# Kernel tuning notes

Hardware: AMD Instinct MI355X
Metric: run time of the kernel (lower is better)

## Reference

```python
import jax, jax.numpy as jnp
import numpy as np

B, T, DIM = 32, 512, 512
Q, C, D = 8, 256, 256   # num_codebooks, nb_code, bottleneck_dim
HID = 1024
EPS = 1e-5


def _bn(h, gamma, beta):
    # BatchNorm1d (training mode): batch stats over all leading dims, biased var
    ax = tuple(range(h.ndim - 1))
    m = h.mean(axis=ax, keepdims=True)
    v = ((h - m) ** 2).mean(axis=ax, keepdims=True)
    return (h - m) / jnp.sqrt(v + EPS) * gamma + beta


def setup_inputs() -> dict:
    key = jax.random.key(0)
    ks = jax.random.split(key, 12)
    s = 0.02  # weight scale
    return {
        "x": jax.random.normal(ks[0], (B, DIM, T), jnp.float32),
        "u": jax.random.uniform(ks[1], (B, T, Q, C), jnp.float32),
        "codebook": jax.random.normal(ks[2], (Q, C, D), jnp.float32),
        "log_temps": jnp.zeros((Q,), jnp.float32),
        "enc_w0": jax.random.normal(ks[3], (HID, DIM), jnp.float32) * s,
        "enc_b0": jnp.zeros((HID,), jnp.float32),
        "enc_g0": jnp.ones((HID,), jnp.float32),
        "enc_be0": jnp.zeros((HID,), jnp.float32),
        "enc_w1": jax.random.normal(ks[4], (HID, HID), jnp.float32) * s,
        "enc_b1": jnp.zeros((HID,), jnp.float32),
        "enc_g1": jnp.ones((HID,), jnp.float32),
        "enc_be1": jnp.zeros((HID,), jnp.float32),
        "enc_wo": jax.random.normal(ks[5], (Q * D, HID), jnp.float32) * s,
        "enc_bo": jnp.zeros((Q * D,), jnp.float32),
        "dec_g": jnp.ones((D,), jnp.float32),
        "dec_be": jnp.zeros((D,), jnp.float32),
        "dec_w0": jax.random.normal(ks[6], (HID, D), jnp.float32) * s,
        "dec_b0": jnp.zeros((HID,), jnp.float32),
        "dec_g0": jnp.ones((HID,), jnp.float32),
        "dec_be0": jnp.zeros((HID,), jnp.float32),
        "dec_w1": jax.random.normal(ks[7], (HID, HID), jnp.float32) * s,
        "dec_b1": jnp.zeros((HID,), jnp.float32),
        "dec_g1": jnp.ones((HID,), jnp.float32),
        "dec_be1": jnp.zeros((HID,), jnp.float32),
        "fin_w": jax.random.normal(ks[8], (DIM, HID), jnp.float32) * s,
        "fin_b": jnp.zeros((DIM,), jnp.float32),
    }


def reference(x, u, codebook, log_temps,
              enc_w0, enc_b0, enc_g0, enc_be0,
              enc_w1, enc_b1, enc_g1, enc_be1,
              enc_wo, enc_bo,
              dec_g, dec_be,
              dec_w0, dec_b0, dec_g0, dec_be0,
              dec_w1, dec_b1, dec_g1, dec_be1,
              fin_w, fin_b):
    xt = jnp.swapaxes(x, 1, 2)  # b c t -> b t c

    # encoder: FFN(dim->hid->hid) + Linear(hid, Q*D)
    h = jax.nn.relu(_bn(xt @ enc_w0.T + enc_b0, enc_g0, enc_be0))
    h = jax.nn.relu(_bn(h @ enc_w1.T + enc_b1, enc_g1, enc_be1))
    z = (h @ enc_wo.T + enc_bo).reshape(B, T, Q, D)

    # multi-codebook logits
    logits_raw = jnp.einsum('btqd,qcd->btqc', z, codebook)  # [B,T,Q,C]
    indices = jnp.argmax(logits_raw, axis=-1)               # [B,T,Q]

    # per-codebook temperature scaling
    logits = logits_raw * jnp.exp(-log_temps)[:, None]

    # gumbel-softmax (tau=1, hard=True), gumbel noise from uniform u
    g = -jnp.log(-jnp.log(jnp.clip(u, 1e-9, 1.0)) + 1e-20)
    y_soft = jax.nn.softmax(logits + g, axis=-1)
    y_hard = jax.nn.one_hot(jnp.argmax(y_soft, axis=-1), C, dtype=y_soft.dtype)
    codes = y_hard - jax.lax.stop_gradient(y_soft) + y_soft  # straight-through

    # decoder: embed via codebook, batchnorm, FFN, final linear
    emb = codes.reshape(B, T, Q * C) @ codebook.reshape(Q * C, D)
    h = _bn(emb, dec_g, dec_be)
    h = jax.nn.relu(_bn(h @ dec_w0.T + dec_b0, dec_g0, dec_be0))
    h = jax.nn.relu(_bn(h @ dec_w1.T + dec_b1, dec_g1, dec_be1))
    x_reco = h @ fin_w.T + fin_b  # [B,T,DIM]

    commit_loss = jnp.mean((x_reco - xt) ** 2)
    return x_reco, indices, commit_loss
```

## Files before the change

kernel.cpp:

```cpp
#include <hip/hip_runtime.h>
#include <math.h>

#define BB   32
#define TT   512
#define DIM  512
#define HID  1024
#define QQ   8
#define CC   256
#define DD   256
#define BT   16384
#define EPSB 1e-5f

typedef _Float16 half4 __attribute__((ext_vector_type(4)));
typedef _Float16 half8 __attribute__((ext_vector_type(8)));
typedef float f32x4 __attribute__((ext_vector_type(4)));

#define GLOAD_LDS16(g, l)                                                      \
  __builtin_amdgcn_global_load_lds(                                            \
      (const __attribute__((address_space(1))) void*)(g),                      \
      (__attribute__((address_space(3))) void*)(l), 16, 0, 0)

__device__ inline void xcd_swizzle(int& bx, int& by) {
  int gx = gridDim.x, gy = gridDim.y;
  int h = blockIdx.x + gx * blockIdx.y;
  int c = h & 7, idx = h >> 3;
  bx = idx % gx;
  by = c * (gy >> 3) + idx / gx;
}

__global__ __launch_bounds__(256) void transpose_xt(const float* __restrict__ x,
                                                    float* __restrict__ xt,
                                                    _Float16* __restrict__ xhi,
                                                    _Float16* __restrict__ xlo) {
  __shared__ float tile[32][33];
  int tx = threadIdx.x, ty = threadIdx.y;
  int b = blockIdx.z;
  int t0 = blockIdx.x * 32, c0 = blockIdx.y * 32;
  const float* xb = x + (size_t)b * DIM * TT;
#pragma unroll
  for (int j = 0; j < 32; j += 8)
    tile[ty + j][tx] = xb[(size_t)(c0 + ty + j) * TT + (t0 + tx)];
  __syncthreads();
#pragma unroll
  for (int j = 0; j < 32; j += 8) {
    float v = tile[tx][ty + j];
    size_t gi = ((size_t)b * TT + t0 + ty + j) * DIM + (c0 + tx);
    xt[gi] = v;
    _Float16 h = (_Float16)v;
    xhi[gi] = h;
    xlo[gi] = (_Float16)(v - (float)h);
  }
}

__device__ inline void conv4(const float* __restrict__ in,
                             _Float16* __restrict__ o, int i) {
  float4 v = ((const float4*)in)[i];
  half4 hv;
  hv.x = (_Float16)v.x; hv.y = (_Float16)v.y;
  hv.z = (_Float16)v.z; hv.w = (_Float16)v.w;
  ((half4*)o)[i] = hv;
}

__device__ inline void split4(const float* __restrict__ in,
                              _Float16* __restrict__ hi,
                              _Float16* __restrict__ lo, int i, float scale) {
  float4 v = ((const float4*)in)[i];
  v.x *= scale; v.y *= scale; v.z *= scale; v.w *= scale;
  half4 hv, lv;
  hv.x = (_Float16)v.x; lv.x = (_Float16)(v.x - (float)hv.x);
  hv.y = (_Float16)v.y; lv.y = (_Float16)(v.y - (float)hv.y);
  hv.z = (_Float16)v.z; lv.z = (_Float16)(v.z - (float)hv.z);
  hv.w = (_Float16)v.w; lv.w = (_Float16)(v.w - (float)hv.w);
  ((half4*)hi)[i] = hv;
  ((half4*)lo)[i] = lv;
}

__global__ __launch_bounds__(256) void prep_weights(
    const float* __restrict__ dw0, const float* __restrict__ dw1,
    const float* __restrict__ fw, const float* __restrict__ ew0,
    const float* __restrict__ ew1, _Float16* __restrict__ w0h,
    _Float16* __restrict__ w1h, _Float16* __restrict__ wfh,
    _Float16* __restrict__ w0hi, _Float16* __restrict__ w0lo,
    _Float16* __restrict__ w1hi, _Float16* __restrict__ w1lo) {
  int b = blockIdx.x, t = threadIdx.x;
  if (b < 256) {
    conv4(dw0, w0h, b * 256 + t);
  } else if (b < 1280) {
    conv4(dw1, w1h, (b - 256) * 256 + t);
  } else if (b < 1792) {
    conv4(fw, wfh, (b - 1280) * 256 + t);
  } else if (b < 2304) {
    split4(ew0, w0hi, w0lo, (b - 1792) * 256 + t, 64.f);
  } else {
    split4(ew1, w1hi, w1lo, (b - 2304) * 256 + t, 64.f);
  }
}

__global__ __launch_bounds__(256) void fold_w(const float* __restrict__ cb,
                                              const float* __restrict__ wo,
                                              float* __restrict__ Wf) {
  __shared__ float As[8][128];
  __shared__ float Ws[8][128];
  const int tid = threadIdx.x;
  const int n0 = blockIdx.x * 128;
  const int m0 = blockIdx.y * 128;
  const int q = m0 >> 8;
  const int lr = tid >> 1, lk = (tid & 1) << 2;
  const float* Ap = cb + (size_t)q * CC * DD + (size_t)((m0 & 255) + lr) * DD + lk;
  const int br = tid >> 5, bc = (tid & 31) << 2;
  const float* Bp = wo + (size_t)(q * CC + br) * HID + n0 + bc;
  const int tm = (tid >> 4) << 3, tn = (tid & 15) << 3;

  float acc[8][8];
#pragma unroll
  for (int i = 0; i < 8; i++)
#pragma unroll
    for (int j = 0; j < 8; j++) acc[i][j] = 0.f;

  for (int kb = 0; kb < DD; kb += 8) {
    float4 av = *(const float4*)(Ap + kb);
    float4 bb = *(const float4*)(Bp + (size_t)kb * HID);
    __syncthreads();
    As[lk + 0][lr] = av.x; As[lk + 1][lr] = av.y;
    As[lk + 2][lr] = av.z; As[lk + 3][lr] = av.w;
    *(float4*)&Ws[br][bc] = bb;
    __syncthreads();
#pragma unroll
    for (int k = 0; k < 8; ++k) {
      float a[8], b[8];
      *(float4*)(a) = *(const float4*)(&As[k][tm]);
      *(float4*)(a + 4) = *(const float4*)(&As[k][tm + 4]);
      *(float4*)(b) = *(const float4*)(&Ws[k][tn]);
      *(float4*)(b + 4) = *(const float4*)(&Ws[k][tn + 4]);
#pragma unroll
      for (int i = 0; i < 8; i++)
#pragma unroll
        for (int j = 0; j < 8; j++) acc[i][j] = fmaf(a[i], b[j], acc[i][j]);
    }
  }
#pragma unroll
  for (int i = 0; i < 8; i++) {
    float* Cp = Wf + (size_t)(m0 + tm + i) * HID + (n0 + tn);
    float4 o;
    o.x = acc[i][0]; o.y = acc[i][1]; o.z = acc[i][2]; o.w = acc[i][3];
    *(float4*)Cp = o;
    o.x = acc[i][4]; o.y = acc[i][5]; o.z = acc[i][6]; o.w = acc[i][7];
    *(float4*)(Cp + 4) = o;
  }
}

__global__ __launch_bounds__(256) void fold_b(const float* __restrict__ cb,
                                              const float* __restrict__ bo,
                                              float* __restrict__ bf) {
  int q = blockIdx.x, c = threadIdx.x;
  const float* row = cb + ((size_t)q * CC + c) * DD;
  const float* b = bo + q * DD;
  float s = 0.f;
  for (int d = 0; d < DD; d++) s = fmaf(row[d], b[d], s);
  bf[q * CC + c] = s;
}

__global__ __launch_bounds__(256, 2) void hgemm3s_nt(
    const _Float16* __restrict__ Ahi, const _Float16* __restrict__ Alo,
    const _Float16* __restrict__ Whi, const _Float16* __restrict__ Wlo,
    const float* __restrict__ bias, float invsc, _Float16* __restrict__ Chi,
    _Float16* __restrict__ Clo, int ldc, int K, float* __restrict__ stats,
    int N) {
  __shared__ _Float16 Ah[4 * 128 * 8];
  __shared__ _Float16 Al[4 * 128 * 8];
  __shared__ _Float16 Bh[4 * 128 * 8];
  __shared__ _Float16 Bl[4 * 128 * 8];
  int BX, BY;
  xcd_swizzle(BX, BY);
  const int tid = threadIdx.x;
  const int l = tid & 63;
  const int w = tid >> 6;
  const int m0 = BY * 128, n0 = BX * 128;
  const int wrow = (w >> 1) * 64, wcol = (w & 1) * 64;

  const int s0 = tid, s1 = tid + 256;
  const int r0 = s0 & 127, kp0 = s0 >> 7;
  const int r1 = s1 & 127, kp1 = s1 >> 7;
  const size_t a0o = (size_t)(m0 + r0) * K + kp0 * 8;
  const size_t a1o = (size_t)(m0 + r1) * K + kp1 * 8;
  const size_t w0o = (size_t)(n0 + r0) * K + kp0 * 8;
  const size_t w1o = (size_t)(n0 + r1) * K + kp1 * 8;

  f32x4 acc[4][4] = {};

  for (int kb = 0; kb < K; kb += 32) {
    __syncthreads();
    GLOAD_LDS16(Ahi + a0o + kb, &Ah[s0 * 8]);
    GLOAD_LDS16(Ahi + a1o + kb, &Ah[s1 * 8]);
    GLOAD_LDS16(Alo + a0o + kb, &Al[s0 * 8]);
    GLOAD_LDS16(Alo + a1o + kb, &Al[s1 * 8]);
    GLOAD_LDS16(Whi + w0o + kb, &Bh[s0 * 8]);
    GLOAD_LDS16(Whi + w1o + kb, &Bh[s1 * 8]);
    GLOAD_LDS16(Wlo + w0o + kb, &Bl[s0 * 8]);
    GLOAD_LDS16(Wlo + w1o + kb, &Bl[s1 * 8]);
    __syncthreads();
    half8 ah[4], al[4], bh[4], bl[4];
#pragma unroll
    for (int i = 0; i < 4; i++) {
      const int idx = (((l >> 4) << 7) + wrow + i * 16 + (l & 15)) * 8;
      ah[i] = *(const half8*)&Ah[idx];
      al[i] = *(const half8*)&Al[idx];
    }
#pragma unroll
    for (int j = 0; j < 4; j++) {
      const int idx = (((l >> 4) << 7) + wcol + j * 16 + (l & 15)) * 8;
      bh[j] = *(const half8*)&Bh[idx];
      bl[j] = *(const half8*)&Bl[idx];
    }
#pragma unroll
    for (int i = 0; i < 4; i++)
#pragma unroll
      for (int j = 0; j < 4; j++) {
        acc[i][j] = __builtin_amdgcn_mfma_f32_16x16x32_f16(ah[i], bh[j],
                                                           acc[i][j], 0, 0, 0);
        acc[i][j] = __builtin_amdgcn_mfma_f32_16x16x32_f16(al[i], bh[j],
                                                           acc[i][j], 0, 0, 0);
        acc[i][j] = __builtin_amdgcn_mfma_f32_16x16x32_f16(ah[i], bl[j],
                                                           acc[i][j], 0, 0, 0);
      }
  }

#pragma unroll
  for (int j = 0; j < 4; j++) {
    const int col = n0 + wcol + j * 16 + (l & 15);
    const float bb = bias[col];
    float s1v = 0.f, s2v = 0.f;
#pragma unroll
    for (int i = 0; i < 4; i++) {
#pragma unroll
      for (int r = 0; r < 4; r++) {
        float v = fmaf(acc[i][j][r], invsc, bb);
        const int row = m0 + wrow + i * 16 + ((l >> 4) << 2) + r;
        _Float16 hv = (_Float16)v;
        Chi[(size_t)row * ldc + col] = hv;
        Clo[(size_t)row * ldc + col] = (_Float16)(v - (float)hv);
        s1v += v;
        s2v = fmaf(v, v, s2v);
      }
    }
    s1v += __shfl_xor(s1v, 16); s1v += __shfl_xor(s1v, 32);
    s2v += __shfl_xor(s2v, 16); s2v += __shfl_xor(s2v, 32);
    if (l < 16) {
      atomicAdd(&stats[col], s1v);
      atomicAdd(&stats[N + col], s2v);
    }
  }
}

__global__ __launch_bounds__(512, 4) void hgemm3_wo_argmax(
    const _Float16* __restrict__ Ahi, const _Float16* __restrict__ Alo,
    const _Float16* __restrict__ Whi, const _Float16* __restrict__ Wlo,
    const float* __restrict__ bf, const float* __restrict__ u,
    const float* __restrict__ log_temps, float* __restrict__ out_idx,
    int* __restrict__ idx2) {
  __shared__ _Float16 Ahs[4 * 128 * 8];
  __shared__ _Float16 Als[4 * 128 * 8];
  __shared__ _Float16 Bhs[4 * 256 * 8];
  __shared__ _Float16 Bls[4 * 256 * 8];
  __shared__ float redv[2][128][4];
  __shared__ int   redi[2][128][4];
  int BX, BY;
  xcd_swizzle(BX, BY);
  const int tid = threadIdx.x;
  const int l = tid & 63;
  const int w = tid >> 6;
  const int q = BX;
  const int m0 = BY * 128;
  const int n0 = q * CC;
  const int wrow = (w >> 2) * 64, wcol = (w & 3) * 64;

  const int ar = tid & 127, akp = tid >> 7;
  const _Float16* Agh = Ahi + (size_t)(m0 + ar) * HID + akp * 8;
  const _Float16* Agl = Alo + (size_t)(m0 + ar) * HID + akp * 8;
  _Float16* Ahd = &Ahs[tid * 8];
  _Float16* Ald = &Als[tid * 8];
  const int s0 = tid, s1 = tid + 512;
  const int br0 = s0 & 255, bkp0 = s0 >> 8;
  const int br1 = s1 & 255, bkp1 = s1 >> 8;
  const _Float16* Bgh0 = Whi + (size_t)(n0 + br0) * HID + bkp0 * 8;
  const _Float16* Bgh1 = Whi + (size_t)(n0 + br1) * HID + bkp1 * 8;
  const _Float16* Bgl0 = Wlo + (size_t)(n0 + br0) * HID + bkp0 * 8;
  const _Float16* Bgl1 = Wlo + (size_t)(n0 + br1) * HID + bkp1 * 8;
  _Float16* Bhd0 = &Bhs[s0 * 8]; _Float16* Bhd1 = &Bhs[s1 * 8];
  _Float16* Bld0 = &Bls[s0 * 8]; _Float16* Bld1 = &Bls[s1 * 8];

  f32x4 acc[4][4] = {};

  for (int kb = 0; kb < HID; kb += 32) {
    __syncthreads();
    GLOAD_LDS16(Agh + kb, Ahd);
    GLOAD_LDS16(Agl + kb, Ald);
    GLOAD_LDS16(Bgh0 + kb, Bhd0);
    GLOAD_LDS16(Bgh1 + kb, Bhd1);
    GLOAD_LDS16(Bgl0 + kb, Bld0);
    GLOAD_LDS16(Bgl1 + kb, Bld1);
    __syncthreads();
    half8 ah[4], al[4], bh[4], bl[4];
#pragma unroll
    for (int i = 0; i < 4; i++) {
      const int idx = ((l >> 4) * 128 + wrow + i * 16 + (l & 15)) * 8;
      ah[i] = *(const half8*)&Ahs[idx];
      al[i] = *(const half8*)&Als[idx];
    }
#pragma unroll
    for (int j = 0; j < 4; j++) {
      const int idx = ((l >> 4) * 256 + wcol + j * 16 + (l & 15)) * 8;
      bh[j] = *(const half8*)&Bhs[idx];
      bl[j] = *(const half8*)&Bls[idx];
    }
#pragma unroll
    for (int i = 0; i < 4; i++)
#pragma unroll
      for (int j = 0; j < 4; j++) {
        acc[i][j] = __builtin_amdgcn_mfma_f32_16x16x32_f16(ah[i], bh[j],
                                                           acc[i][j], 0, 0, 0);
        acc[i][j] = __builtin_amdgcn_mfma_f32_16x16x32_f16(al[i], bh[j],
                                                           acc[i][j], 0, 0, 0);
        acc[i][j] = __builtin_amdgcn_mfma_f32_16x16x32_f16(ah[i], bl[j],
                                                           acc[i][j], 0, 0, 0);
      }
  }

  const float scale = expf(-log_temps[q]);
  float bcol[4];
#pragma unroll
  for (int j = 0; j < 4; j++) bcol[j] = bf[n0 + wcol + j * 16 + (l & 15)];

#pragma unroll
  for (int i = 0; i < 4; i++) {
#pragma unroll
    for (int r = 0; r < 4; r++) {
      const int rloc = wrow + i * 16 + ((l >> 4) << 2) + r;
      const int row = m0 + rloc;
      float bvv = -INFINITY; int bi = 0;
      float gv = -INFINITY; int gi = 0;
#pragma unroll
      for (int j = 0; j < 4; j++) {
        const int c = wcol + j * 16 + (l & 15);
        float v = acc[i][j][r] + bcol[j];
        if (v > bvv) { bvv = v; bi = c; }
        float uu = u[(size_t)row * (QQ * CC) + n0 + c];
        float uc = fminf(fmaxf(uu, 1e-9f), 1.0f);
        float g = -logf(-logf(uc) + 1e-20f);
        float y = fmaf(v, scale, g);
        if (y > gv) { gv = y; gi = c; }
      }
#pragma unroll
      for (int off = 1; off < 16; off <<= 1) {
        float b2 = __shfl_xor(bvv, off); int bi2 = __shfl_xor(bi, off);
        if (b2 > bvv || (b2 == bvv && bi2 < bi)) { bvv = b2; bi = bi2; }
        float g2 = __shfl_xor(gv, off); int gi2 = __shfl_xor(gi, off);
        if (g2 > gv || (g2 == gv && gi2 < gi)) { gv = g2; gi = gi2; }
      }
      if ((l & 15) == 0) {
        redv[0][rloc][w & 3] = bvv; redi[0][rloc][w & 3] = bi;
        redv[1][rloc][w & 3] = gv;  redi[1][rloc][w & 3] = gi;
      }
    }
  }
  __syncthreads();
  if (tid < 128) {
    float bv = redv[0][tid][0]; int bi = redi[0][tid][0];
    float gv = redv[1][tid][0]; int gi = redi[1][tid][0];
#pragma unroll
    for (int c = 1; c < 4; c++) {
      float v = redv[0][tid][c];
      if (v > bv) { bv = v; bi = redi[0][tid][c]; }
      float v2 = redv[1][tid][c];
      if (v2 > gv) { gv = v2; gi = redi[1][tid][c]; }
    }
    const int row = m0 + tid;
    out_idx[(size_t)row * QQ + q] = (float)bi;
    idx2[(size_t)row * QQ + q] = gi;
  }
}

__global__ __launch_bounds__(256, 2) void hgemm_ntf16(
    const _Float16* __restrict__ A, const _Float16* __restrict__ W,
    const float* __restrict__ bias, _Float16* __restrict__ C, int ldc, int K,
    float* __restrict__ stats, int N) {
  __shared__ _Float16 Al[4 * 128 * 8];
  __shared__ _Float16 Bl[4 * 128 * 8];
  int BX, BY;
  xcd_swizzle(BX, BY);
  const int tid = threadIdx.x;
  const int l = tid & 63;
  const int w = tid >> 6;
  const int m0 = BY * 128, n0 = BX * 128;
  const int wrow = (w >> 1) * 64, wcol = (w & 1) * 64;

  const int s0 = tid, s1 = tid + 256;
  const int r0 = s0 & 127, kp0 = s0 >> 7;
  const int r1 = s1 & 127, kp1 = s1 >> 7;
  const _Float16* Ag0 = A + (size_t)(m0 + r0) * K + kp0 * 8;
  const _Float16* Ag1 = A + (size_t)(m0 + r1) * K + kp1 * 8;
  const _Float16* Wg0 = W + (size_t)(n0 + r0) * K + kp0 * 8;
  const _Float16* Wg1 = W + (size_t)(n0 + r1) * K + kp1 * 8;
  _Float16* Al0 = &Al[s0 * 8]; _Float16* Al1 = &Al[s1 * 8];
  _Float16* Bl0 = &Bl[s0 * 8]; _Float16* Bl1 = &Bl[s1 * 8];

  f32x4 acc[4][4] = {};

  for (int kb = 0; kb < K; kb += 32) {
    __syncthreads();
    GLOAD_LDS16(Ag0 + kb, Al0);
    GLOAD_LDS16(Ag1 + kb, Al1);
    GLOAD_LDS16(Wg0 + kb, Bl0);
    GLOAD_LDS16(Wg1 + kb, Bl1);
    __syncthreads();
    half8 af[4], bf[4];
#pragma unroll
    for (int i = 0; i < 4; i++)
      af[i] = *(const half8*)&Al[(((l >> 4) << 7) + wrow + i * 16 + (l & 15)) * 8];
#pragma unroll
    for (int j = 0; j < 4; j++)
      bf[j] = *(const half8*)&Bl[(((l >> 4) << 7) + wcol + j * 16 + (l & 15)) * 8];
#pragma unroll
    for (int i = 0; i < 4; i++)
#pragma unroll
      for (int j = 0; j < 4; j++)
        acc[i][j] = __builtin_amdgcn_mfma_f32_16x16x32_f16(af[i], bf[j],
                                                           acc[i][j], 0, 0, 0);
  }

#pragma unroll
  for (int j = 0; j < 4; j++) {
    const int col = n0 + wcol + j * 16 + (l & 15);
    const float bb = bias[col];
    float s1v = 0.f, s2v = 0.f;
#pragma unroll
    for (int i = 0; i < 4; i++) {
#pragma unroll
      for (int r = 0; r < 4; r++) {
        float v = acc[i][j][r] + bb;
        const int row = m0 + wrow + i * 16 + ((l >> 4) << 2) + r;
        C[(size_t)row * ldc + col] = (_Float16)v;
        s1v += v;
        s2v = fmaf(v, v, s2v);
      }
    }
    s1v += __shfl_xor(s1v, 16); s1v += __shfl_xor(s1v, 32);
    s2v += __shfl_xor(s2v, 16); s2v += __shfl_xor(s2v, 32);
    if (l < 16) {
      atomicAdd(&stats[col], s1v);
      atomicAdd(&stats[N + col], s2v);
    }
  }
}

__global__ __launch_bounds__(256, 2) void hgemm_nt_loss(
    const _Float16* __restrict__ A, const _Float16* __restrict__ W,
    const float* __restrict__ bias, float* __restrict__ C, int ldc, int K,
    const float* __restrict__ xt, float* __restrict__ out_loss) {
  __shared__ _Float16 Al[4 * 128 * 8];
  __shared__ _Float16 Bl[4 * 128 * 8];
  int BX, BY;
  xcd_swizzle(BX, BY);
  const int tid = threadIdx.x;
  const int l = tid & 63;
  const int w = tid >> 6;
  const int m0 = BY * 128, n0 = BX * 128;
  const int wrow = (w >> 1) * 64, wcol = (w & 1) * 64;

  const int s0 = tid, s1 = tid + 256;
  const int r0 = s0 & 127, kp0 = s0 >> 7;
  const int r1 = s1 & 127, kp1 = s1 >> 7;
  const _Float16* Ag0 = A + (size_t)(m0 + r0) * K + kp0 * 8;
  const _Float16* Ag1 = A + (size_t)(m0 + r1) * K + kp1 * 8;
  const _Float16* Wg0 = W + (size_t)(n0 + r0) * K + kp0 * 8;
  const _Float16* Wg1 = W + (size_t)(n0 + r1) * K + kp1 * 8;
  _Float16* Al0 = &Al[s0 * 8]; _Float16* Al1 = &Al[s1 * 8];
  _Float16* Bl0 = &Bl[s0 * 8]; _Float16* Bl1 = &Bl[s1 * 8];

  f32x4 acc[4][4] = {};

  for (int kb = 0; kb < K; kb += 32) {
    __syncthreads();
    GLOAD_LDS16(Ag0 + kb, Al0);
    GLOAD_LDS16(Ag1 + kb, Al1);
    GLOAD_LDS16(Wg0 + kb, Bl0);
    GLOAD_LDS16(Wg1 + kb, Bl1);
    __syncthreads();
    half8 af[4], bf[4];
#pragma unroll
    for (int i = 0; i < 4; i++)
      af[i] = *(const half8*)&Al[(((l >> 4) << 7) + wrow + i * 16 + (l & 15)) * 8];
#pragma unroll
    for (int j = 0; j < 4; j++)
      bf[j] = *(const half8*)&Bl[(((l >> 4) << 7) + wcol + j * 16 + (l & 15)) * 8];
#pragma unroll
    for (int i = 0; i < 4; i++)
#pragma unroll
      for (int j = 0; j < 4; j++)
        acc[i][j] = __builtin_amdgcn_mfma_f32_16x16x32_f16(af[i], bf[j],
                                                           acc[i][j], 0, 0, 0);
  }

  float ls = 0.f;
#pragma unroll
  for (int j = 0; j < 4; j++) {
    const int col = n0 + wcol + j * 16 + (l & 15);
    const float bb = bias[col];
#pragma unroll
    for (int i = 0; i < 4; i++) {
#pragma unroll
      for (int r = 0; r < 4; r++) {
        float v = acc[i][j][r] + bb;
        const int row = m0 + wrow + i * 16 + ((l >> 4) << 2) + r;
        C[(size_t)row * ldc + col] = v;
        float d = v - xt[(size_t)row * ldc + col];
        ls = fmaf(d, d, ls);
      }
    }
  }
#pragma unroll
  for (int off = 32; off > 0; off >>= 1) ls += __shfl_xor(ls, off);
  if (l == 0)
    atomicAdd(out_loss, ls * (1.0f / ((float)BT * (float)DIM)));
}

__global__ __launch_bounds__(256) void bn_finalize(const float* __restrict__ sums,
                                                   const float* __restrict__ gamma,
                                                   const float* __restrict__ beta,
                                                   float* __restrict__ ss, int N) {
  int n = blockIdx.x * 256 + threadIdx.x;
  if (n >= N) return;
  const float invM = 1.0f / (float)BT;
  float mean = sums[n] * invM;
  float var = sums[N + n] * invM - mean * mean;
  float sc = gamma[n] / sqrtf(var + EPSB);
  ss[n] = sc;
  ss[N + n] = beta[n] - mean * sc;
}

__global__ __launch_bounds__(256) void bn_resplit(_Float16* __restrict__ hi,
                                                  _Float16* __restrict__ lo,
                                                  const float* __restrict__ ss,
                                                  int nmask, int N, long n4,
                                                  int relu) {
  long stride = (long)gridDim.x * 256;
  for (long i = (long)blockIdx.x * 256 + threadIdx.x; i < n4; i += stride) {
    int col = (int)((i << 2) & nmask);
    half4 h = ((half4*)hi)[i];
    half4 L = ((half4*)lo)[i];
    float4 sc = *(const float4*)(ss + col);
    float4 sh = *(const float4*)(ss + N + col);
    float vx = fmaf((float)h.x + (float)L.x, sc.x, sh.x);
    float vy = fmaf((float)h.y + (float)L.y, sc.y, sh.y);
    float vz = fmaf((float)h.z + (float)L.z, sc.z, sh.z);
    float vw = fmaf((float)h.w + (float)L.w, sc.w, sh.w);
    if (relu) {
      vx = fmaxf(vx, 0.f); vy = fmaxf(vy, 0.f);
      vz = fmaxf(vz, 0.f); vw = fmaxf(vw, 0.f);
    }
    half4 hv, lv;
    hv.x = (_Float16)vx; lv.x = (_Float16)(vx - (float)hv.x);
    hv.y = (_Float16)vy; lv.y = (_Float16)(vy - (float)hv.y);
    hv.z = (_Float16)vz; lv.z = (_Float16)(vz - (float)hv.z);
    hv.w = (_Float16)vw; lv.w = (_Float16)(vw - (float)hv.w);
    ((half4*)hi)[i] = hv;
    ((half4*)lo)[i] = lv;
  }
}

__global__ __launch_bounds__(256) void bnf16_inplace(_Float16* __restrict__ h,
                                                     const float* __restrict__ ss,
                                                     int nmask, int N, long n4,
                                                     int relu) {
  long stride = (long)gridDim.x * 256;
  for (long i = (long)blockIdx.x * 256 + threadIdx.x; i < n4; i += stride) {
    int col = (int)((i << 2) & nmask);
    half4 v = ((half4*)h)[i];
    float4 sc = *(const float4*)(ss + col);
    float4 sh = *(const float4*)(ss + N + col);
    float vx = fmaf((float)v.x, sc.x, sh.x);
    float vy = fmaf((float)v.y, sc.y, sh.y);
    float vz = fmaf((float)v.z, sc.z, sh.z);
    float vw = fmaf((float)v.w, sc.w, sh.w);
    if (relu) {
      vx = fmaxf(vx, 0.f); vy = fmaxf(vy, 0.f);
      vz = fmaxf(vz, 0.f); vw = fmaxf(vw, 0.f);
    }
    half4 o;
    o.x = (_Float16)vx; o.y = (_Float16)vy;
    o.z = (_Float16)vz; o.w = (_Float16)vw;
    ((half4*)h)[i] = o;
  }
}

__global__ __launch_bounds__(256) void bn_apply_f16(const float* __restrict__ h,
                                                    const float* __restrict__ ss,
                                                    int nmask, int N, long n4,
                                                    int relu,
                                                    _Float16* __restrict__ o) {
  long stride = (long)gridDim.x * 256;
  for (long i = (long)blockIdx.x * 256 + threadIdx.x; i < n4; i += stride) {
    int col = (int)((i << 2) & nmask);
    float4 v = ((const float4*)h)[i];
    float4 sc = *(const float4*)(ss + col);
    float4 sh = *(const float4*)(ss + N + col);
    v.x = fmaf(v.x, sc.x, sh.x); v.y = fmaf(v.y, sc.y, sh.y);
    v.z = fmaf(v.z, sc.z, sh.z); v.w = fmaf(v.w, sc.w, sh.w);
    if (relu) {
      v.x = fmaxf(v.x, 0.f); v.y = fmaxf(v.y, 0.f);
      v.z = fmaxf(v.z, 0.f); v.w = fmaxf(v.w, 0.f);
    }
    half4 hv;
    hv.x = (_Float16)v.x; hv.y = (_Float16)v.y;
    hv.z = (_Float16)v.z; hv.w = (_Float16)v.w;
    ((half4*)o)[i] = hv;
  }
}

__global__ __launch_bounds__(256) void conv_split_s(const float* __restrict__ in,
                                                    _Float16* __restrict__ hi,
                                                    _Float16* __restrict__ lo,
                                                    int n4, float scale) {
  int i = blockIdx.x * 256 + threadIdx.x;
  if (i >= n4) return;
  split4(in, hi, lo, i, scale);
}

__global__ __launch_bounds__(256) void emb_gather_stats(
    const float* __restrict__ cb, const int* __restrict__ idx2,
    float* __restrict__ emb, float* __restrict__ sums) {
  __shared__ int k[64][8];
  const int r0 = blockIdx.x * 64;
  const int tid = threadIdx.x;
  for (int t = tid; t < 64 * QQ; t += 256)
    k[t >> 3][t & 7] = idx2[(size_t)(r0 + (t >> 3)) * QQ + (t & 7)];
  __syncthreads();
  const int d = tid;
  float s1 = 0.f, s2 = 0.f;
  for (int rr = 0; rr < 64; rr++) {
    float s = 0.f;
#pragma unroll
    for (int q = 0; q < QQ; q++)
      s += cb[((size_t)(q * CC + k[rr][q])) * DD + d];
    emb[(size_t)(r0 + rr) * DD + d] = s;
    s1 += s;
    s2 = fmaf(s, s, s2);
  }
  atomicAdd(&sums[d], s1);
  atomicAdd(&sums[DD + d], s2);
}

static const size_t OF_XT = 0;
static const size_t OF_R1 = OF_XT + (size_t)BT * DIM;
static const size_t OF_R2 = OF_R1 + (size_t)BT * HID;
static const size_t OF_WF = OF_R2 + (size_t)BT * HID;
static const size_t OF_BF = OF_WF + (size_t)2048 * HID;
static const size_t OF_EMBH = OF_BF + 2048;
static const size_t OF_HB = OF_EMBH + (size_t)BT * DD / 2;
static const size_t OF_W0H = OF_HB + (size_t)BT * HID / 2;
static const size_t OF_W1H = OF_W0H + (size_t)HID * DD / 2;
static const size_t OF_WFH = OF_W1H + (size_t)HID * HID / 2;
static const size_t OF_I2 = OF_WFH + (size_t)DIM * HID / 2;
static const size_t OF_ST = OF_I2 + (size_t)BT * QQ;
static const size_t OF_SS0 = OF_ST + 4096;
static const size_t OF_SS1 = OF_SS0 + 2048;
static const size_t OF_SSD = OF_SS1 + 2048;
static const size_t OF_SD0 = OF_SSD + 1024;
static const size_t OF_SD1 = OF_SD0 + 2048;

extern "C" void kernel_launch(void* const* d_in, const int* in_sizes, int n_in,
                              void* d_out, int out_size, void* d_ws, size_t ws_size,
                              hipStream_t stream) {
  const float* x        = (const float*)d_in[0];
  const float* u        = (const float*)d_in[1];
  const float* codebook = (const float*)d_in[2];
  const float* log_temps= (const float*)d_in[3];
  const float* enc_w0   = (const float*)d_in[4];
  const float* enc_b0   = (const float*)d_in[5];
  const float* enc_g0   = (const float*)d_in[6];
  const float* enc_be0  = (const float*)d_in[7];
  const float* enc_w1   = (const float*)d_in[8];
  const float* enc_b1   = (const float*)d_in[9];
  const float* enc_g1   = (const float*)d_in[10];
  const float* enc_be1  = (const float*)d_in[11];
  const float* enc_wo   = (const float*)d_in[12];
  const float* enc_bo   = (const float*)d_in[13];
  const float* dec_g    = (const float*)d_in[14];
  const float* dec_be   = (const float*)d_in[15];
  const float* dec_w0   = (const float*)d_in[16];
  const float* dec_b0   = (const float*)d_in[17];
  const float* dec_g0   = (const float*)d_in[18];
  const float* dec_be0  = (const float*)d_in[19];
  const float* dec_w1   = (const float*)d_in[20];
  const float* dec_b1   = (const float*)d_in[21];
  const float* dec_g1   = (const float*)d_in[22];
  const float* dec_be1  = (const float*)d_in[23];
  const float* fin_w    = (const float*)d_in[24];
  const float* fin_b    = (const float*)d_in[25];

  float* ws = (float*)d_ws;
  float* xt = ws + OF_XT;
  float* R1 = ws + OF_R1;
  float* Wf = ws + OF_WF;
  float* bfold = ws + OF_BF;
  _Float16* embh = (_Float16*)(ws + OF_EMBH);
  _Float16* w0h = (_Float16*)(ws + OF_W0H);
  _Float16* w1h = (_Float16*)(ws + OF_W1H);
  _Float16* wfh = (_Float16*)(ws + OF_WFH);
  int* idx2 = (int*)(ws + OF_I2);
  float* st = ws + OF_ST;
  float* ss0 = ws + OF_SS0;
  float* ss1 = ws + OF_SS1;
  float* ssd = ws + OF_SSD;
  float* sd0 = ws + OF_SD0;
  float* sd1 = ws + OF_SD1;

  _Float16* xthi = (_Float16*)(ws + OF_R2);
  _Float16* xtlo = (_Float16*)(ws + OF_R2 + (size_t)BT * DIM / 2);
  _Float16* w0hi = (_Float16*)(ws + OF_R2 + (size_t)BT * DIM);
  _Float16* w0lo = (_Float16*)(ws + OF_R2 + (size_t)BT * DIM + (size_t)HID * DIM / 2);
  _Float16* w1hi = (_Float16*)(ws + OF_R2 + (size_t)BT * DIM + (size_t)HID * DIM);
  _Float16* w1lo = (_Float16*)(ws + OF_R2 + (size_t)BT * DIM + (size_t)HID * DIM +
                               (size_t)HID * HID / 2);
  _Float16* r1hi = (_Float16*)(ws + OF_R1);
  _Float16* r1lo = (_Float16*)(ws + OF_R1 + (size_t)BT * HID / 2);
  _Float16* r2hi = (_Float16*)(ws + OF_HB);
  _Float16* r2lo = (_Float16*)(ws + OF_R2);
  _Float16* wfhi = (_Float16*)(ws + OF_R1);
  _Float16* wflo = (_Float16*)(ws + OF_R1 + (size_t)2048 * HID / 2);
  _Float16* h16a = (_Float16*)(ws + OF_R2);
  _Float16* h16b = (_Float16*)(ws + OF_R2 + (size_t)BT * HID / 2);

  float* out = (float*)d_out;
  float* out_idx = out + (size_t)BT * DIM;
  float* out_loss = out + (size_t)BT * DIM + (size_t)BT * QQ;

  hipMemsetAsync(out_loss, 0, sizeof(float), stream);

  prep_weights<<<dim3(3328), 256, 0, stream>>>(
      dec_w0, dec_w1, fin_w, enc_w0, enc_w1, w0h, w1h, wfh, w0hi, w0lo, w1hi,
      w1lo);
  fold_w<<<dim3(HID / 128, 2048 / 128), 256, 0, stream>>>(codebook, enc_wo, Wf);
  fold_b<<<dim3(QQ), 256, 0, stream>>>(codebook, enc_bo, bfold);

  transpose_xt<<<dim3(TT / 32, DIM / 32, BB), dim3(32, 8), 0, stream>>>(
      x, xt, xthi, xtlo);

  hipMemsetAsync(st, 0, 2 * HID * sizeof(float), stream);
  hgemm3s_nt<<<dim3(HID / 128, BT / 128), 256, 0, stream>>>(
      xthi, xtlo, w0hi, w0lo, enc_b0, 1.f / 64.f, r1hi, r1lo, HID, DIM, st, HID);
  bn_finalize<<<dim3(4), 256, 0, stream>>>(st, enc_g0, enc_be0, ss0, HID);
  bn_resplit<<<dim3(2048), 256, 0, stream>>>(r1hi, r1lo, ss0, HID - 1, HID,
                                             (long)BT * HID / 4, 1);

  hipMemsetAsync(st, 0, 2 * HID * sizeof(float), stream);
  hgemm3s_nt<<<dim3(HID / 128, BT / 128), 256, 0, stream>>>(
      r1hi, r1lo, w1hi, w1lo, enc_b1, 1.f / 64.f, r2hi, r2lo, HID, HID, st, HID);
  conv_split_s<<<dim3(2048 * HID / 4 / 256), 256, 0, stream>>>(
      Wf, wfhi, wflo, 2048 * HID / 4, 1.f);
  bn_finalize<<<dim3(4), 256, 0, stream>>>(st, enc_g1, enc_be1, ss1, HID);
  bn_resplit<<<dim3(2048), 256, 0, stream>>>(r2hi, r2lo, ss1, HID - 1, HID,
                                             (long)BT * HID / 4, 1);

  hgemm3_wo_argmax<<<dim3(QQ, BT / 128), 512, 0, stream>>>(
      r2hi, r2lo, wfhi, wflo, bfold, u, log_temps, out_idx, idx2);

  hipMemsetAsync(st, 0, 2 * DD * sizeof(float), stream);
  emb_gather_stats<<<dim3(BT / 64), 256, 0, stream>>>(codebook, idx2, R1, st);
  bn_finalize<<<dim3(1), 256, 0, stream>>>(st, dec_g, dec_be, ssd, DD);
  bn_apply_f16<<<dim3(2048), 256, 0, stream>>>(R1, ssd, DD - 1, DD,
                                               (long)BT * DD / 4, 0, embh);

  hipMemsetAsync(st, 0, 2 * HID * sizeof(float), stream);
  hgemm_ntf16<<<dim3(HID / 128, BT / 128), 256, 0, stream>>>(
      embh, w0h, dec_b0, h16a, HID, DD, st, HID);
  bn_finalize<<<dim3(4), 256, 0, stream>>>(st, dec_g0, dec_be0, sd0, HID);
  bnf16_inplace<<<dim3(2048), 256, 0, stream>>>(h16a, sd0, HID - 1, HID,
                                                (long)BT * HID / 4, 1);

  hipMemsetAsync(st, 0, 2 * HID * sizeof(float), stream);
  hgemm_ntf16<<<dim3(HID / 128, BT / 128), 256, 0, stream>>>(
      h16a, w1h, dec_b1, h16b, HID, HID, st, HID);
  bn_finalize<<<dim3(4), 256, 0, stream>>>(st, dec_g1, dec_be1, sd1, HID);
  bnf16_inplace<<<dim3(2048), 256, 0, stream>>>(h16b, sd1, HID - 1, HID,
                                                (long)BT * HID / 4, 1);

  hgemm_nt_loss<<<dim3(DIM / 128, BT / 128), 256, 0, stream>>>(
      h16b, wfh, fin_b, out, DIM, HID, xt, out_loss);
}
```

Measured before the change: 1.180 ms.

## Double-buffer LDS tiles in fp16 GEMMs to overlap global loads with MFMA

Converts three GEMM kernels (the split-precision 3-pass GEMM, the stats GEMM and the final loss GEMM) from a single-buffered load-sync-compute loop to a two-stage ping-pong LDS pipeline. The next K-slab is issued with global_load_lds before computing the current one, and explicit s_waitcnt vmcnt plus s_barrier wait only for the older batch. The aim is to hide global memory latency behind the MFMA work. The cost is twice the LDS per block, up to 64KB in the 3-pass kernel, which can reduce occupancy. The hand-written waitcnt values must also match the number of loads in flight.

```diff
diff --git a/kernel.cpp b/kernel.cpp
--- a/kernel.cpp
+++ b/kernel.cpp
@@ -19,6 +19,11 @@
   __builtin_amdgcn_global_load_lds(                                            \
       (const __attribute__((address_space(1))) void*)(g),                      \
       (__attribute__((address_space(3))) void*)(l), 16, 0, 0)
+
+#define S_BARRIER() asm volatile("s_barrier" ::: "memory")
+#define S_VMCNT8()  asm volatile("s_waitcnt vmcnt(8)" ::: "memory")
+#define S_VMCNT4()  asm volatile("s_waitcnt vmcnt(4)" ::: "memory")
+#define S_VMCNT0()  asm volatile("s_waitcnt vmcnt(0)" ::: "memory")
 
 __device__ inline void xcd_swizzle(int& bx, int& by) {
   int gx = gridDim.x, gy = gridDim.y;
@@ -166,10 +171,10 @@
     const float* __restrict__ bias, float invsc, _Float16* __restrict__ Chi,
     _Float16* __restrict__ Clo, int ldc, int K, float* __restrict__ stats,
     int N) {
-  __shared__ _Float16 Ah[4 * 128 * 8];
-  __shared__ _Float16 Al[4 * 128 * 8];
-  __shared__ _Float16 Bh[4 * 128 * 8];
-  __shared__ _Float16 Bl[4 * 128 * 8];
+  __shared__ _Float16 Ah[2][4 * 128 * 8];
+  __shared__ _Float16 Al[2][4 * 128 * 8];
+  __shared__ _Float16 Bh[2][4 * 128 * 8];
+  __shared__ _Float16 Bl[2][4 * 128 * 8];
   int BX, BY;
   xcd_swizzle(BX, BY);
   const int tid = threadIdx.x;
@@ -188,29 +193,29 @@
 
   f32x4 acc[4][4] = {};
 
-  for (int kb = 0; kb < K; kb += 32) {
-    __syncthreads();
-    GLOAD_LDS16(Ahi + a0o + kb, &Ah[s0 * 8]);
-    GLOAD_LDS16(Ahi + a1o + kb, &Ah[s1 * 8]);
-    GLOAD_LDS16(Alo + a0o + kb, &Al[s0 * 8]);
-    GLOAD_LDS16(Alo + a1o + kb, &Al[s1 * 8]);
-    GLOAD_LDS16(Whi + w0o + kb, &Bh[s0 * 8]);
-    GLOAD_LDS16(Whi + w1o + kb, &Bh[s1 * 8]);
-    GLOAD_LDS16(Wlo + w0o + kb, &Bl[s0 * 8]);
-    GLOAD_LDS16(Wlo + w1o + kb, &Bl[s1 * 8]);
-    __syncthreads();
+  auto stage = [&](int buf, int kb) {
+    GLOAD_LDS16(Ahi + a0o + kb, &Ah[buf][s0 * 8]);
+    GLOAD_LDS16(Ahi + a1o + kb, &Ah[buf][s1 * 8]);
+    GLOAD_LDS16(Alo + a0o + kb, &Al[buf][s0 * 8]);
+    GLOAD_LDS16(Alo + a1o + kb, &Al[buf][s1 * 8]);
+    GLOAD_LDS16(Whi + w0o + kb, &Bh[buf][s0 * 8]);
+    GLOAD_LDS16(Whi + w1o + kb, &Bh[buf][s1 * 8]);
+    GLOAD_LDS16(Wlo + w0o + kb, &Bl[buf][s0 * 8]);
+    GLOAD_LDS16(Wlo + w1o + kb, &Bl[buf][s1 * 8]);
+  };
+  auto compute = [&](int buf) {
     half8 ah[4], al[4], bh[4], bl[4];
 #pragma unroll
     for (int i = 0; i < 4; i++) {
       const int idx = (((l >> 4) << 7) + wrow + i * 16 + (l & 15)) * 8;
-      ah[i] = *(const half8*)&Ah[idx];
-      al[i] = *(const half8*)&Al[idx];
+      ah[i] = *(const half8*)&Ah[buf][idx];
+      al[i] = *(const half8*)&Al[buf][idx];
     }
 #pragma unroll
     for (int j = 0; j < 4; j++) {
       const int idx = (((l >> 4) << 7) + wcol + j * 16 + (l & 15)) * 8;
-      bh[j] = *(const half8*)&Bh[idx];
-      bl[j] = *(const half8*)&Bl[idx];
+      bh[j] = *(const half8*)&Bh[buf][idx];
+      bl[j] = *(const half8*)&Bl[buf][idx];
     }
 #pragma unroll
     for (int i = 0; i < 4; i++)
@@ -223,7 +228,21 @@
         acc[i][j] = __builtin_amdgcn_mfma_f32_16x16x32_f16(ah[i], bl[j],
                                                            acc[i][j], 0, 0, 0);
       }
-  }
+  };
+
+  stage(0, 0);
+  int cur = 0;
+  for (int kb = 32; kb < K; kb += 32) {
+    stage(cur ^ 1, kb);
+    S_VMCNT8();
+    S_BARRIER();
+    compute(cur);
+    S_BARRIER();
+    cur ^= 1;
+  }
+  S_VMCNT0();
+  S_BARRIER();
+  compute(cur);
 
 #pragma unroll
   for (int j = 0; j < 4; j++) {
@@ -384,8 +403,8 @@
     const _Float16* __restrict__ A, const _Float16* __restrict__ W,
     const float* __restrict__ bias, _Float16* __restrict__ C, int ldc, int K,
     float* __restrict__ stats, int N) {
-  __shared__ _Float16 Al[4 * 128 * 8];
-  __shared__ _Float16 Bl[4 * 128 * 8];
+  __shared__ _Float16 Al[2][4 * 128 * 8];
+  __shared__ _Float16 Bl[2][4 * 128 * 8];
   int BX, BY;
   xcd_swizzle(BX, BY);
   const int tid = threadIdx.x;
@@ -397,36 +416,50 @@
   const int s0 = tid, s1 = tid + 256;
   const int r0 = s0 & 127, kp0 = s0 >> 7;
   const int r1 = s1 & 127, kp1 = s1 >> 7;
-  const _Float16* Ag0 = A + (size_t)(m0 + r0) * K + kp0 * 8;
-  const _Float16* Ag1 = A + (size_t)(m0 + r1) * K + kp1 * 8;
-  const _Float16* Wg0 = W + (size_t)(n0 + r0) * K + kp0 * 8;
-  const _Float16* Wg1 = W + (size_t)(n0 + r1) * K + kp1 * 8;
-  _Float16* Al0 = &Al[s0 * 8]; _Float16* Al1 = &Al[s1 * 8];
-  _Float16* Bl0 = &Bl[s0 * 8]; _Float16* Bl1 = &Bl[s1 * 8];
+  const size_t a0o = (size_t)(m0 + r0) * K + kp0 * 8;
+  const size_t a1o = (size_t)(m0 + r1) * K + kp1 * 8;
+  const size_t w0o = (size_t)(n0 + r0) * K + kp0 * 8;
+  const size_t w1o = (size_t)(n0 + r1) * K + kp1 * 8;
 
   f32x4 acc[4][4] = {};
 
-  for (int kb = 0; kb < K; kb += 32) {
-    __syncthreads();
-    GLOAD_LDS16(Ag0 + kb, Al0);
-    GLOAD_LDS16(Ag1 + kb, Al1);
-    GLOAD_LDS16(Wg0 + kb, Bl0);
-    GLOAD_LDS16(Wg1 + kb, Bl1);
-    __syncthreads();
-    half8 af[4], bf[4];
+  auto stage = [&](int buf, int kb) {
+    GLOAD_LDS16(A + a0o + kb, &Al[buf][s0 * 8]);
+    GLOAD_LDS16(A + a1o + kb, &Al[buf][s1 * 8]);
+    GLOAD_LDS16(W + w0o + kb, &Bl[buf][s0 * 8]);
+    GLOAD_LDS16(W + w1o + kb, &Bl[buf][s1 * 8]);
+  };
+  auto compute = [&](int buf) {
+    half8 af[4], bfr[4];
 #pragma unroll
     for (int i = 0; i < 4; i++)
-      af[i] = *(const half8*)&Al[(((l >> 4) << 7) + wrow + i * 16 + (l & 15)) * 8];
+      af[i] = *(const half8*)
+          &Al[buf][(((l >> 4) << 7) + wrow + i * 16 + (l & 15)) * 8];
 #pragma unroll
     for (int j = 0; j < 4; j++)
-      bf[j] = *(const half8*)&Bl[(((l >> 4) << 7) + wcol + j * 16 + (l & 15)) * 8];
+      bfr[j] = *(const half8*)
+          &Bl[buf][(((l >> 4) << 7) + wcol + j * 16 + (l & 15)) * 8];
 #pragma unroll
     for (int i = 0; i < 4; i++)
 #pragma unroll
       for (int j = 0; j < 4; j++)
-        acc[i][j] = __builtin_amdgcn_mfma_f32_16x16x32_f16(af[i], bf[j],
+        acc[i][j] = __builtin_amdgcn_mfma_f32_16x16x32_f16(af[i], bfr[j],
                                                            acc[i][j], 0, 0, 0);
-  }
+  };
+
+  stage(0, 0);
+  int cur = 0;
+  for (int kb = 32; kb < K; kb += 32) {
+    stage(cur ^ 1, kb);
+    S_VMCNT4();
+    S_BARRIER();
+    compute(cur);
+    S_BARRIER();
+    cur ^= 1;
+  }
+  S_VMCNT0();
+  S_BARRIER();
+  compute(cur);
 
 #pragma unroll
   for (int j = 0; j < 4; j++) {
@@ -457,8 +490,8 @@
     const _Float16* __restrict__ A, const _Float16* __restrict__ W,
     const float* __restrict__ bias, float* __restrict__ C, int ldc, int K,
     const float* __restrict__ xt, float* __restrict__ out_loss) {
-  __shared__ _Float16 Al[4 * 128 * 8];
-  __shared__ _Float16 Bl[4 * 128 * 8];
+  __shared__ _Float16 Al[2][4 * 128 * 8];
+  __shared__ _Float16 Bl[2][4 * 128 * 8];
   int BX, BY;
   xcd_swizzle(BX, BY);
   const int tid = threadIdx.x;
@@ -470,36 +503,50 @@
   const int s0 = tid, s1 = tid + 256;
   const int r0 = s0 & 127, kp0 = s0 >> 7;
   const int r1 = s1 & 127, kp1 = s1 >> 7;
-  const _Float16* Ag0 = A + (size_t)(m0 + r0) * K + kp0 * 8;
-  const _Float16* Ag1 = A + (size_t)(m0 + r1) * K + kp1 * 8;
-  const _Float16* Wg0 = W + (size_t)(n0 + r0) * K + kp0 * 8;
-  const _Float16* Wg1 = W + (size_t)(n0 + r1) * K + kp1 * 8;
-  _Float16* Al0 = &Al[s0 * 8]; _Float16* Al1 = &Al[s1 * 8];
-  _Float16* Bl0 = &Bl[s0 * 8]; _Float16* Bl1 = &Bl[s1 * 8];
+  const size_t a0o = (size_t)(m0 + r0) * K + kp0 * 8;
+  const size_t a1o = (size_t)(m0 + r1) * K + kp1 * 8;
+  const size_t w0o = (size_t)(n0 + r0) * K + kp0 * 8;
+  const size_t w1o = (size_t)(n0 + r1) * K + kp1 * 8;
 
   f32x4 acc[4][4] = {};
 
-  for (int kb = 0; kb < K; kb += 32) {
-    __syncthreads();
-    GLOAD_LDS16(Ag0 + kb, Al0);
-    GLOAD_LDS16(Ag1 + kb, Al1);
-    GLOAD_LDS16(Wg0 + kb, Bl0);
-    GLOAD_LDS16(Wg1 + kb, Bl1);
-    __syncthreads();
-    half8 af[4], bf[4];
+  auto stage = [&](int buf, int kb) {
+    GLOAD_LDS16(A + a0o + kb, &Al[buf][s0 * 8]);
+    GLOAD_LDS16(A + a1o + kb, &Al[buf][s1 * 8]);
+    GLOAD_LDS16(W + w0o + kb, &Bl[buf][s0 * 8]);
+    GLOAD_LDS16(W + w1o + kb, &Bl[buf][s1 * 8]);
+  };
+  auto compute = [&](int buf) {
+    half8 af[4], bfr[4];
 #pragma unroll
     for (int i = 0; i < 4; i++)
-      af[i] = *(const half8*)&Al[(((l >> 4) << 7) + wrow + i * 16 + (l & 15)) * 8];
+      af[i] = *(const half8*)
+          &Al[buf][(((l >> 4) << 7) + wrow + i * 16 + (l & 15)) * 8];
 #pragma unroll
     for (int j = 0; j < 4; j++)
-      bf[j] = *(const half8*)&Bl[(((l >> 4) << 7) + wcol + j * 16 + (l & 15)) * 8];
+      bfr[j] = *(const half8*)
+          &Bl[buf][(((l >> 4) << 7) + wcol + j * 16 + (l & 15)) * 8];
 #pragma unroll
     for (int i = 0; i < 4; i++)
 #pragma unroll
       for (int j = 0; j < 4; j++)
-        acc[i][j] = __builtin_amdgcn_mfma_f32_16x16x32_f16(af[i], bf[j],
+        acc[i][j] = __builtin_amdgcn_mfma_f32_16x16x32_f16(af[i], bfr[j],
                                                            acc[i][j], 0, 0, 0);
-  }
+  };
+
+  stage(0, 0);
+  int cur = 0;
+  for (int kb = 32; kb < K; kb += 32) {
+    stage(cur ^ 1, kb);
+    S_VMCNT4();
+    S_BARRIER();
+    compute(cur);
+    S_BARRIER();
+    cur ^= 1;
+  }
+  S_VMCNT0();
+  S_BARRIER();
+  compute(cur);
 
   float ls = 0.f;
 #pragma unroll
```

Result: no change. 1.163 ms, median of 2 (-1.4%).
